# Kernel optimization log

Measured on AMD Instinct MI355X. Metric: run time of the kernel, lower is better.

## Reference

```python
import jax, jax.numpy as jnp
import numpy as np

N_NODES = 100000
N_EDGES = 1250000
D = 64


def _sage_conv(x, src, dst, W_l, b_l, W_r, n_nodes):
    # message = x[src]; scatter-mean onto dst; then lin_l(mean) + lin_r(x)
    msg = x[src]                                               # [E, D]
    agg = jax.ops.segment_sum(msg, dst, num_segments=n_nodes)  # [N, D]
    cnt = jax.ops.segment_sum(jnp.ones((src.shape[0],), x.dtype), dst,
                              num_segments=n_nodes)            # [N]
    mean = agg / jnp.maximum(cnt, 1.0)[:, None]
    return mean @ W_l + b_l + x @ W_r


def setup_inputs() -> dict:
    key = jax.random.key(0)
    ks = jax.random.split(key, 8)
    s = 1.0 / np.sqrt(D)
    x = jax.random.normal(ks[0], (N_NODES, D), dtype=jnp.float32)
    edge_index = jax.random.randint(ks[1], (2, N_EDGES), 0, N_NODES, dtype=jnp.int32)
    W_l1 = jax.random.normal(ks[2], (D, D), dtype=jnp.float32) * s
    b_l1 = jnp.zeros((D,), jnp.float32)
    W_r1 = jax.random.normal(ks[3], (D, D), dtype=jnp.float32) * s
    W_l2 = jax.random.normal(ks[4], (D, D), dtype=jnp.float32) * s
    b_l2 = jnp.zeros((D,), jnp.float32)
    W_r2 = jax.random.normal(ks[5], (D, D), dtype=jnp.float32) * s
    return {"x": x, "edge_index": edge_index,
            "W_l1": W_l1, "b_l1": b_l1, "W_r1": W_r1,
            "W_l2": W_l2, "b_l2": b_l2, "W_r2": W_r2}


def reference(x, edge_index, W_l1, b_l1, W_r1, W_l2, b_l2, W_r2):
    src, dst = edge_index[0], edge_index[1]
    n = x.shape[0]
    h = jax.nn.relu(_sage_conv(x, src, dst, W_l1, b_l1, W_r1, n))
    return _sage_conv(h, src, dst, W_l2, b_l2, W_r2, n)
```

## Files before the change

kernel.cpp:

```cpp
#include <hip/hip_runtime.h>

#define N_NODES 100000
#define N_EDGES 1250000
#define D 64

#define BIN_SHIFT 9
#define BIN_NODES 512
#define NBINS ((N_NODES + BIN_NODES - 1) >> BIN_SHIFT)
#define BIN_CAP 7168
#define SLAB 8704
#define CHUNK 4096
#define ZERO_NODE N_NODES

typedef __attribute__((ext_vector_type(8))) short short8;
typedef __attribute__((ext_vector_type(4))) float f32x4;

__device__ inline unsigned short f2bf(float f) {
    unsigned int u = __float_as_uint(f);
    unsigned int r = (u + 0x7fffu + ((u >> 16) & 1u)) >> 16;
    return (unsigned short)r;
}
__device__ inline float4 unpack_bf4(uint2 u) {
    float4 f;
    f.x = __uint_as_float(u.x << 16);
    f.y = __uint_as_float(u.x & 0xffff0000u);
    f.z = __uint_as_float(u.y << 16);
    f.w = __uint_as_float(u.y & 0xffff0000u);
    return f;
}

__global__ __launch_bounds__(256)
void convert_zero_kernel(const float4* __restrict__ xin, ushort4* __restrict__ xb,
                         int n4, int* __restrict__ bin_cnt,
                         unsigned int* __restrict__ xb_zrow,
                         unsigned int* __restrict__ h_zrow,
                         const float* __restrict__ Wl1, const float* __restrict__ Wr1,
                         const float* __restrict__ Wl2, const float* __restrict__ Wr2,
                         unsigned short* __restrict__ wt) {
    int i = blockIdx.x * 256 + threadIdx.x;
    if (i < n4) {
        float4 v = xin[i];
        ushort4 u;
        u.x = f2bf(v.x); u.y = f2bf(v.y); u.z = f2bf(v.z); u.w = f2bf(v.w);
        xb[i] = u;
    }
    if (i < NBINS) bin_cnt[i] = 0;
    if (i < 32) { xb_zrow[i] = 0u; h_zrow[i] = 0u; }
    if (i < 2 * 64 * 128) {
        int layer = i >> 13;
        int n = (i >> 7) & 63;
        int k = i & 127;
        const float* W = layer ? (k < 64 ? Wl2 : Wr2) : (k < 64 ? Wl1 : Wr1);
        float v = W[(k & 63) * D + n];
        wt[i] = f2bf(v);
    }
}

__global__ __launch_bounds__(256)
void bin_kernel(const int* __restrict__ src, const int* __restrict__ dst,
                int* __restrict__ bin_cnt, int* __restrict__ slabs) {
    __shared__ int lhist[NBINS];
    __shared__ int lstart[NBINS];
    __shared__ int lbase[NBINS];
    __shared__ int lcur[NBINS];
    __shared__ int pscan[256];
    __shared__ int sval[CHUNK];
    __shared__ int sdst[CHUNK];

    const int t = threadIdx.x;
    const int e0 = blockIdx.x * CHUNK;
    int cnt = N_EDGES - e0; if (cnt > CHUNK) cnt = CHUNK;

    for (int i = t; i < NBINS; i += 256) lhist[i] = 0;
    __syncthreads();

    for (int i = t; i < cnt; i += 256)
        atomicAdd(&lhist[dst[e0 + i] >> BIN_SHIFT], 1);
    __syncthreads();

    int h = (t < NBINS) ? lhist[t] : 0;
    pscan[t] = h;
    __syncthreads();
    for (int off = 1; off < 256; off <<= 1) {
        int x = (t >= off) ? pscan[t - off] : 0;
        __syncthreads();
        pscan[t] += x;
        __syncthreads();
    }
    if (t < NBINS) {
        int excl = pscan[t] - h;
        lstart[t] = excl;
        lcur[t] = excl;
        lbase[t] = (h > 0) ? atomicAdd(&bin_cnt[t], h) : 0;
    }
    __syncthreads();

    for (int i = t; i < cnt; i += 256) {
        int d = dst[e0 + i];
        int s = src[e0 + i];
        int b = d >> BIN_SHIFT;
        int slot = atomicAdd(&lcur[b], 1);
        int rank = slot - lstart[b];
        sval[slot] = (s << BIN_SHIFT) | (d & (BIN_NODES - 1));
        int gp = lbase[b] + rank;
        sdst[slot] = (gp < BIN_CAP) ? (b * SLAB + gp) : -1;
    }
    __syncthreads();

    for (int i = t; i < cnt; i += 256) {
        int dd = sdst[i];
        if (dd >= 0) slabs[dd] = sval[i];
    }
}

__global__ __launch_bounds__(256)
void bin_sort_kernel(int* __restrict__ slabs, const int* __restrict__ bin_cnt,
                     int* __restrict__ deg_out, int* __restrict__ rstart_out) {
    __shared__ int hist[BIN_NODES];
    __shared__ int cur[BIN_NODES];
    __shared__ int pscan[256];
    __shared__ int stage[BIN_CAP];

    const int b = blockIdx.x;
    const int t = threadIdx.x;
    int cnt = bin_cnt[b]; if (cnt > BIN_CAP) cnt = BIN_CAP;
    const int nb0 = b << BIN_SHIFT;
    const int nn = (N_NODES - nb0 < BIN_NODES) ? (N_NODES - nb0) : BIN_NODES;
    const int slab0 = b * SLAB;

    hist[t] = 0; hist[t + 256] = 0;
    __syncthreads();

    for (int i = t; i < cnt; i += 256) {
        int p = slabs[slab0 + i];
        stage[i] = p;
        atomicAdd(&hist[p & (BIN_NODES - 1)], 1);
    }
    __syncthreads();

    int h0 = hist[2 * t], h1 = hist[2 * t + 1];
    int ph0 = (h0 + 3) & ~3, ph1 = (h1 + 3) & ~3;
    int pv = ph0 + ph1;
    pscan[t] = pv;
    __syncthreads();
    for (int off = 1; off < 256; off <<= 1) {
        int x = (t >= off) ? pscan[t - off] : 0;
        __syncthreads();
        pscan[t] += x;
        __syncthreads();
    }
    int pairExcl = pscan[t] - pv;
    int s0 = pairExcl, s1 = pairExcl + ph0;
    cur[2 * t] = s0;
    cur[2 * t + 1] = s1;
    if (2 * t < nn) {
        deg_out[nb0 + 2 * t] = h0;
        rstart_out[nb0 + 2 * t] = slab0 + s0;
        for (int i = h0; i < ph0; ++i) slabs[slab0 + s0 + i] = ZERO_NODE;
    }
    if (2 * t + 1 < nn) {
        deg_out[nb0 + 2 * t + 1] = h1;
        rstart_out[nb0 + 2 * t + 1] = slab0 + s1;
        for (int i = h1; i < ph1; ++i) slabs[slab0 + s1 + i] = ZERO_NODE;
    }
    __syncthreads();

    for (int i = t; i < cnt; i += 256) {
        int p = stage[i];
        int pos = atomicAdd(&cur[p & (BIN_NODES - 1)], 1);
        slabs[slab0 + pos] = p >> BIN_SHIFT;
    }
}

template <typename TOUT>
__global__ __launch_bounds__(256, 8)
void fused_layer_kernel(const unsigned short* __restrict__ xin,
                        const int* __restrict__ rstart,
                        const int* __restrict__ deg,
                        const int* __restrict__ sorted_src,
                        const unsigned short* __restrict__ wt,
                        const float* __restrict__ bl,
                        TOUT* __restrict__ out,
                        int relu) {
    __shared__ __align__(16) unsigned short sA[32][136];

    const uint2* __restrict__ xin64 = (const uint2*)xin;

    const int tid = threadIdx.x;
    const int row0 = blockIdx.x * 32;

    const int wave = tid >> 6;
    const int lane = tid & 63;
    const int q  = lane >> 4;
    const int f2 = lane & 15;

    for (int r = wave; r < 32; r += 4) {
        int n = row0 + r;
        float4 a = make_float4(0.f, 0.f, 0.f, 0.f);
        int dg = deg[n];
        int pdg = (dg + 3) & ~3;
        int st = rstart[n];
        uint2 xraw = xin64[(size_t)n * 16 + f2];

        for (int base = 0; base < pdg; base += 64) {
            int m = pdg - base; if (m > 64) m = 64;
            int idx = 0;
            if (lane < m) idx = sorted_src[st + base + lane];
            int quads = m >> 2;
            float4 c0 = make_float4(0.f, 0.f, 0.f, 0.f);
            float4 c1 = make_float4(0.f, 0.f, 0.f, 0.f);
            float4 c2 = make_float4(0.f, 0.f, 0.f, 0.f);
            float4 c3 = make_float4(0.f, 0.f, 0.f, 0.f);
            int t = 0;
            for (; t + 4 <= quads; t += 4) {
                int sA_ = __shfl(idx, 4 * t + q);
                int sB_ = __shfl(idx, 4 * t + 4 + q);
                int sC_ = __shfl(idx, 4 * t + 8 + q);
                int sD_ = __shfl(idx, 4 * t + 12 + q);
                float4 fA = unpack_bf4(xin64[(size_t)sA_ * 16 + f2]);
                float4 fB = unpack_bf4(xin64[(size_t)sB_ * 16 + f2]);
                float4 fC = unpack_bf4(xin64[(size_t)sC_ * 16 + f2]);
                float4 fD = unpack_bf4(xin64[(size_t)sD_ * 16 + f2]);
                c0.x += fA.x; c0.y += fA.y; c0.z += fA.z; c0.w += fA.w;
                c1.x += fB.x; c1.y += fB.y; c1.z += fB.z; c1.w += fB.w;
                c2.x += fC.x; c2.y += fC.y; c2.z += fC.z; c2.w += fC.w;
                c3.x += fD.x; c3.y += fD.y; c3.z += fD.z; c3.w += fD.w;
            }
            for (; t + 2 <= quads; t += 2) {
                int sA_ = __shfl(idx, 4 * t + q);
                int sB_ = __shfl(idx, 4 * t + 4 + q);
                float4 fA = unpack_bf4(xin64[(size_t)sA_ * 16 + f2]);
                float4 fB = unpack_bf4(xin64[(size_t)sB_ * 16 + f2]);
                c0.x += fA.x; c0.y += fA.y; c0.z += fA.z; c0.w += fA.w;
                c1.x += fB.x; c1.y += fB.y; c1.z += fB.z; c1.w += fB.w;
            }
            for (; t < quads; ++t) {
                int sA_ = __shfl(idx, 4 * t + q);
                float4 fA = unpack_bf4(xin64[(size_t)sA_ * 16 + f2]);
                c0.x += fA.x; c0.y += fA.y; c0.z += fA.z; c0.w += fA.w;
            }
            a.x += (c0.x + c1.x) + (c2.x + c3.x);
            a.y += (c0.y + c1.y) + (c2.y + c3.y);
            a.z += (c0.z + c1.z) + (c2.z + c3.z);
            a.w += (c0.w + c1.w) + (c2.w + c3.w);
        }

        a.x += __shfl_xor(a.x, 16); a.y += __shfl_xor(a.y, 16);
        a.z += __shfl_xor(a.z, 16); a.w += __shfl_xor(a.w, 16);
        a.x += __shfl_xor(a.x, 32); a.y += __shfl_xor(a.y, 32);
        a.z += __shfl_xor(a.z, 32); a.w += __shfl_xor(a.w, 32);

        float inv = 1.0f / (float)(dg > 0 ? dg : 1);
        if (q == 0) {
            unsigned int p0 = (unsigned int)f2bf(a.x * inv) |
                              ((unsigned int)f2bf(a.y * inv) << 16);
            unsigned int p1 = (unsigned int)f2bf(a.z * inv) |
                              ((unsigned int)f2bf(a.w * inv) << 16);
            *(uint2*)&sA[r][f2 * 4] = make_uint2(p0, p1);
            *(uint2*)&sA[r][64 + f2 * 4] = xraw;
        }
    }
    __syncthreads();

    const int tm = wave & 1;
    const int tn0 = (wave >> 1) * 2;
    const int mrow = tm * 16 + (lane & 15);
    const int kq = (lane >> 4) * 8;

    short8 afr[4];
#pragma unroll
    for (int kk = 0; kk < 4; ++kk)
        afr[kk] = *(const short8*)&sA[mrow][kk * 32 + kq];

#pragma unroll
    for (int ti = 0; ti < 2; ++ti) {
        const int tn = tn0 + ti;
        const int col = tn * 16 + (lane & 15);
        float bias = bl[col];
        f32x4 acc = {bias, bias, bias, bias};
#pragma unroll
        for (int kk = 0; kk < 4; ++kk) {
            short8 bfr = *(const short8*)&wt[col * 128 + kk * 32 + kq];
            acc = __builtin_amdgcn_mfma_f32_16x16x32_bf16(afr[kk], bfr, acc, 0, 0, 0);
        }
        const int r0 = row0 + tm * 16 + (lane >> 4) * 4;
#pragma unroll
        for (int reg = 0; reg < 4; ++reg) {
            float o = relu ? fmaxf(acc[reg], 0.f) : acc[reg];
            if constexpr (__hip_internal::is_same<TOUT, unsigned short>::value)
                out[(size_t)(r0 + reg) * D + col] = f2bf(o);
            else
                out[(size_t)(r0 + reg) * D + col] = o;
        }
    }
}

extern "C" void kernel_launch(void* const* d_in, const int* in_sizes, int n_in,
                              void* d_out, int out_size, void* d_ws, size_t ws_size,
                              hipStream_t stream) {
    const float* x   = (const float*)d_in[0];
    const int*   ei  = (const int*)d_in[1];
    const float* Wl1 = (const float*)d_in[2];
    const float* b1  = (const float*)d_in[3];
    const float* Wr1 = (const float*)d_in[4];
    const float* Wl2 = (const float*)d_in[5];
    const float* b2  = (const float*)d_in[6];
    const float* Wr2 = (const float*)d_in[7];

    const int* src = ei;
    const int* dst = ei + N_EDGES;

    int* slabs   = (int*)d_ws;
    int* bin_cnt = slabs + (size_t)NBINS * SLAB;
    int* deg     = bin_cnt + 256;
    int* rstart  = deg + N_NODES;
    unsigned short* wt_all = (unsigned short*)(rstart + N_NODES);
    unsigned short* wt1 = wt_all;
    unsigned short* wt2 = wt_all + 64 * 128;
    unsigned short* h = wt_all + 2 * 64 * 128;
    float* out = (float*)d_out;
    unsigned short* xb = (unsigned short*)d_out;

    const int dense_blocks = N_NODES / 32;
    const int conv4 = N_NODES * D / 4;
    const int bin_blocks = (N_EDGES + CHUNK - 1) / CHUNK;

    convert_zero_kernel<<<(conv4 + 255) / 256, 256, 0, stream>>>(
        (const float4*)x, (ushort4*)xb, conv4, bin_cnt,
        (unsigned int*)(xb + (size_t)ZERO_NODE * D),
        (unsigned int*)(h + (size_t)ZERO_NODE * D),
        Wl1, Wr1, Wl2, Wr2, wt_all);

    bin_kernel<<<bin_blocks, 256, 0, stream>>>(src, dst, bin_cnt, slabs);
    bin_sort_kernel<<<NBINS, 256, 0, stream>>>(slabs, bin_cnt, deg, rstart);

    fused_layer_kernel<unsigned short><<<dense_blocks, 256, 0, stream>>>(
        xb, rstart, deg, slabs, wt1, b1, h, 1);
    fused_layer_kernel<float><<<dense_blocks, 256, 0, stream>>>(
        h, rstart, deg, slabs, wt2, b2, out, 0);
}
```

Baseline: 221.8 us.

## Replace two-pass bin sort with global atomic count, scan, and scatter CSR build

Replaces the shared-memory binning and per-bin sort of edges by destination with a standard CSR build. It counts degrees with global atomics, runs a two-level prefix scan over padded degrees, zero-fills the padding, then scatters sources using per-node atomic cursors. This removes the fixed per-bin capacity limit and the two shared-memory passes, but adds several kernel launches and many contended global atomics. Source order within each node becomes nondeterministic, so floating-point summation order can vary between runs.

```diff
diff --git a/kernel.cpp b/kernel.cpp
--- a/kernel.cpp
+++ b/kernel.cpp
@@ -3,14 +3,12 @@
 #define N_NODES 100000
 #define N_EDGES 1250000
 #define D 64
-
-#define BIN_SHIFT 9
-#define BIN_NODES 512
-#define NBINS ((N_NODES + BIN_NODES - 1) >> BIN_SHIFT)
-#define BIN_CAP 7168
-#define SLAB 8704
-#define CHUNK 4096
 #define ZERO_NODE N_NODES
+
+#define SLAB_INTS 1600000
+
+#define SCAN_BLOCKS 196
+#define SCAN_ELEMS 512
 
 typedef __attribute__((ext_vector_type(8))) short short8;
 typedef __attribute__((ext_vector_type(4))) float f32x4;
@@ -31,7 +29,7 @@
 
 __global__ __launch_bounds__(256)
 void convert_zero_kernel(const float4* __restrict__ xin, ushort4* __restrict__ xb,
-                         int n4, int* __restrict__ bin_cnt,
+                         int n4, int* __restrict__ deg,
                          unsigned int* __restrict__ xb_zrow,
                          unsigned int* __restrict__ h_zrow,
                          const float* __restrict__ Wl1, const float* __restrict__ Wr1,
@@ -44,7 +42,7 @@
         u.x = f2bf(v.x); u.y = f2bf(v.y); u.z = f2bf(v.z); u.w = f2bf(v.w);
         xb[i] = u;
     }
-    if (i < NBINS) bin_cnt[i] = 0;
+    if (i < N_NODES) deg[i] = 0;
     if (i < 32) { xb_zrow[i] = 0u; h_zrow[i] = 0u; }
     if (i < 2 * 64 * 128) {
         int layer = i >> 13;
@@ -57,90 +55,22 @@
 }
 
 __global__ __launch_bounds__(256)
-void bin_kernel(const int* __restrict__ src, const int* __restrict__ dst,
-                int* __restrict__ bin_cnt, int* __restrict__ slabs) {
-    __shared__ int lhist[NBINS];
-    __shared__ int lstart[NBINS];
-    __shared__ int lbase[NBINS];
-    __shared__ int lcur[NBINS];
+void count_kernel(const int* __restrict__ dst, int* __restrict__ deg) {
+    int i = blockIdx.x * 256 + threadIdx.x;
+    if (i < N_EDGES) atomicAdd(&deg[dst[i]], 1);
+}
+
+__global__ __launch_bounds__(256)
+void scan_block_kernel(const int* __restrict__ deg, int* __restrict__ rstart,
+                       int* __restrict__ bsum) {
     __shared__ int pscan[256];
-    __shared__ int sval[CHUNK];
-    __shared__ int sdst[CHUNK];
-
-    const int t = threadIdx.x;
-    const int e0 = blockIdx.x * CHUNK;
-    int cnt = N_EDGES - e0; if (cnt > CHUNK) cnt = CHUNK;
-
-    for (int i = t; i < NBINS; i += 256) lhist[i] = 0;
-    __syncthreads();
-
-    for (int i = t; i < cnt; i += 256)
-        atomicAdd(&lhist[dst[e0 + i] >> BIN_SHIFT], 1);
-    __syncthreads();
-
-    int h = (t < NBINS) ? lhist[t] : 0;
-    pscan[t] = h;
-    __syncthreads();
-    for (int off = 1; off < 256; off <<= 1) {
-        int x = (t >= off) ? pscan[t - off] : 0;
-        __syncthreads();
-        pscan[t] += x;
-        __syncthreads();
-    }
-    if (t < NBINS) {
-        int excl = pscan[t] - h;
-        lstart[t] = excl;
-        lcur[t] = excl;
-        lbase[t] = (h > 0) ? atomicAdd(&bin_cnt[t], h) : 0;
-    }
-    __syncthreads();
-
-    for (int i = t; i < cnt; i += 256) {
-        int d = dst[e0 + i];
-        int s = src[e0 + i];
-        int b = d >> BIN_SHIFT;
-        int slot = atomicAdd(&lcur[b], 1);
-        int rank = slot - lstart[b];
-        sval[slot] = (s << BIN_SHIFT) | (d & (BIN_NODES - 1));
-        int gp = lbase[b] + rank;
-        sdst[slot] = (gp < BIN_CAP) ? (b * SLAB + gp) : -1;
-    }
-    __syncthreads();
-
-    for (int i = t; i < cnt; i += 256) {
-        int dd = sdst[i];
-        if (dd >= 0) slabs[dd] = sval[i];
-    }
-}
-
-__global__ __launch_bounds__(256)
-void bin_sort_kernel(int* __restrict__ slabs, const int* __restrict__ bin_cnt,
-                     int* __restrict__ deg_out, int* __restrict__ rstart_out) {
-    __shared__ int hist[BIN_NODES];
-    __shared__ int cur[BIN_NODES];
-    __shared__ int pscan[256];
-    __shared__ int stage[BIN_CAP];
-
-    const int b = blockIdx.x;
-    const int t = threadIdx.x;
-    int cnt = bin_cnt[b]; if (cnt > BIN_CAP) cnt = BIN_CAP;
-    const int nb0 = b << BIN_SHIFT;
-    const int nn = (N_NODES - nb0 < BIN_NODES) ? (N_NODES - nb0) : BIN_NODES;
-    const int slab0 = b * SLAB;
-
-    hist[t] = 0; hist[t + 256] = 0;
-    __syncthreads();
-
-    for (int i = t; i < cnt; i += 256) {
-        int p = slabs[slab0 + i];
-        stage[i] = p;
-        atomicAdd(&hist[p & (BIN_NODES - 1)], 1);
-    }
-    __syncthreads();
-
-    int h0 = hist[2 * t], h1 = hist[2 * t + 1];
-    int ph0 = (h0 + 3) & ~3, ph1 = (h1 + 3) & ~3;
-    int pv = ph0 + ph1;
+    const int b = blockIdx.x, t = threadIdx.x;
+    const int i0 = b * SCAN_ELEMS + 2 * t;
+    const int i1 = i0 + 1;
+    int d0 = (i0 < N_NODES) ? deg[i0] : 0;
+    int d1 = (i1 < N_NODES) ? deg[i1] : 0;
+    int p0 = (d0 + 3) & ~3, p1 = (d1 + 3) & ~3;
+    int pv = p0 + p1;
     pscan[t] = pv;
     __syncthreads();
     for (int off = 1; off < 256; off <<= 1) {
@@ -149,26 +79,57 @@
         pscan[t] += x;
         __syncthreads();
     }
-    int pairExcl = pscan[t] - pv;
-    int s0 = pairExcl, s1 = pairExcl + ph0;
-    cur[2 * t] = s0;
-    cur[2 * t + 1] = s1;
-    if (2 * t < nn) {
-        deg_out[nb0 + 2 * t] = h0;
-        rstart_out[nb0 + 2 * t] = slab0 + s0;
-        for (int i = h0; i < ph0; ++i) slabs[slab0 + s0 + i] = ZERO_NODE;
-    }
-    if (2 * t + 1 < nn) {
-        deg_out[nb0 + 2 * t + 1] = h1;
-        rstart_out[nb0 + 2 * t + 1] = slab0 + s1;
-        for (int i = h1; i < ph1; ++i) slabs[slab0 + s1 + i] = ZERO_NODE;
-    }
+    int excl = pscan[t] - pv;
+    if (i0 < N_NODES) rstart[i0] = excl;
+    if (i1 < N_NODES) rstart[i1] = excl + p0;
+    if (t == 255) bsum[b] = pscan[255];
+}
+
+__global__ __launch_bounds__(256)
+void scan_top_kernel(const int* __restrict__ bsum, int* __restrict__ boff) {
+    __shared__ int pscan[256];
+    const int t = threadIdx.x;
+    int v = (t < SCAN_BLOCKS) ? bsum[t] : 0;
+    pscan[t] = v;
     __syncthreads();
-
-    for (int i = t; i < cnt; i += 256) {
-        int p = stage[i];
-        int pos = atomicAdd(&cur[p & (BIN_NODES - 1)], 1);
-        slabs[slab0 + pos] = p >> BIN_SHIFT;
+    for (int off = 1; off < 256; off <<= 1) {
+        int x = (t >= off) ? pscan[t - off] : 0;
+        __syncthreads();
+        pscan[t] += x;
+        __syncthreads();
+    }
+    if (t < SCAN_BLOCKS) boff[t] = pscan[t] - v;
+}
+
+__global__ __launch_bounds__(256)
+void finalize_kernel(const int* __restrict__ deg, int* __restrict__ rstart,
+                     const int* __restrict__ boff, int* __restrict__ cur,
+                     int* __restrict__ slabs) {
+    const int b = blockIdx.x, t = threadIdx.x;
+    const int off = boff[b];
+#pragma unroll
+    for (int k = 0; k < 2; ++k) {
+        int i = b * SCAN_ELEMS + t + k * 256;
+        if (i < N_NODES) {
+            int rs = rstart[i] + off;
+            rstart[i] = rs;
+            cur[i] = rs;
+            int dg = deg[i];
+            int pdg = (dg + 3) & ~3;
+            for (int j = dg; j < pdg; ++j) slabs[rs + j] = ZERO_NODE;
+        }
+    }
+}
+
+__global__ __launch_bounds__(256)
+void scatter_kernel(const int* __restrict__ src, const int* __restrict__ dst,
+                    int* __restrict__ cur, int* __restrict__ slabs) {
+    int i = blockIdx.x * 256 + threadIdx.x;
+    if (i < N_EDGES) {
+        int d = dst[i];
+        int s = src[i];
+        int pos = atomicAdd(&cur[d], 1);
+        slabs[pos] = s;
     }
 }
 
@@ -311,10 +272,12 @@
     const int* dst = ei + N_EDGES;
 
     int* slabs   = (int*)d_ws;
-    int* bin_cnt = slabs + (size_t)NBINS * SLAB;
-    int* deg     = bin_cnt + 256;
+    int* deg     = slabs + SLAB_INTS;
     int* rstart  = deg + N_NODES;
-    unsigned short* wt_all = (unsigned short*)(rstart + N_NODES);
+    int* cur     = rstart + N_NODES;
+    int* bsum    = cur + N_NODES;
+    int* boff    = bsum + 256;
+    unsigned short* wt_all = (unsigned short*)(boff + 256);
     unsigned short* wt1 = wt_all;
     unsigned short* wt2 = wt_all + 64 * 128;
     unsigned short* h = wt_all + 2 * 64 * 128;
@@ -323,16 +286,19 @@
 
     const int dense_blocks = N_NODES / 32;
     const int conv4 = N_NODES * D / 4;
-    const int bin_blocks = (N_EDGES + CHUNK - 1) / CHUNK;
+    const int edge_blocks = (N_EDGES + 255) / 256;
 
     convert_zero_kernel<<<(conv4 + 255) / 256, 256, 0, stream>>>(
-        (const float4*)x, (ushort4*)xb, conv4, bin_cnt,
+        (const float4*)x, (ushort4*)xb, conv4, deg,
         (unsigned int*)(xb + (size_t)ZERO_NODE * D),
         (unsigned int*)(h + (size_t)ZERO_NODE * D),
         Wl1, Wr1, Wl2, Wr2, wt_all);
 
-    bin_kernel<<<bin_blocks, 256, 0, stream>>>(src, dst, bin_cnt, slabs);
-    bin_sort_kernel<<<NBINS, 256, 0, stream>>>(slabs, bin_cnt, deg, rstart);
+    count_kernel<<<edge_blocks, 256, 0, stream>>>(dst, deg);
+    scan_block_kernel<<<SCAN_BLOCKS, 256, 0, stream>>>(deg, rstart, bsum);
+    scan_top_kernel<<<1, 256, 0, stream>>>(bsum, boff);
+    finalize_kernel<<<SCAN_BLOCKS, 256, 0, stream>>>(deg, rstart, boff, cur, slabs);
+    scatter_kernel<<<edge_blocks, 256, 0, stream>>>(src, dst, cur, slabs);
 
     fused_layer_kernel<unsigned short><<<dense_blocks, 256, 0, stream>>>(
         xb, rstart, deg, slabs, wt1, b1, h, 1);
```

After: 340.0 us. +53.3%, slower.

## Replace per-bin sort with global degree scan and segmented bin scatter

Applied to the files above, without the earlier changes.

Degrees are now counted with global atomics during binning, then turned into row starts by a two-level prefix scan over all nodes. The single 196-block bin_sort kernel, which used a large shared staging buffer, is replaced by a scatter kernel that runs four blocks per bin, each handling a quarter of the bin's nodes. The aim is more parallelism and occupancy in the CSR build, and a compact global layout for the sorted edge lists. In exchange it adds kernel launches and a global atomic per edge, and each scatter block re-reads the whole bin. The bin staging buffer now lives in the output buffer at an offset, which relies on that space being free at that point.

```diff
diff --git a/kernel.cpp b/kernel.cpp
--- a/kernel.cpp
+++ b/kernel.cpp
@@ -3,14 +3,18 @@
 #define N_NODES 100000
 #define N_EDGES 1250000
 #define D 64
+#define ZERO_NODE N_NODES
 
 #define BIN_SHIFT 9
 #define BIN_NODES 512
 #define NBINS ((N_NODES + BIN_NODES - 1) >> BIN_SHIFT)
 #define BIN_CAP 7168
-#define SLAB 8704
 #define CHUNK 4096
-#define ZERO_NODE N_NODES
+
+#define SLAB_INTS 1600000
+
+#define SCAN_BLOCKS 196
+#define SCAN_ELEMS 512
 
 typedef __attribute__((ext_vector_type(8))) short short8;
 typedef __attribute__((ext_vector_type(4))) float f32x4;
@@ -31,7 +35,7 @@
 
 __global__ __launch_bounds__(256)
 void convert_zero_kernel(const float4* __restrict__ xin, ushort4* __restrict__ xb,
-                         int n4, int* __restrict__ bin_cnt,
+                         int n4, int* __restrict__ deg, int* __restrict__ bin_cnt,
                          unsigned int* __restrict__ xb_zrow,
                          unsigned int* __restrict__ h_zrow,
                          const float* __restrict__ Wl1, const float* __restrict__ Wr1,
@@ -44,6 +48,7 @@
         u.x = f2bf(v.x); u.y = f2bf(v.y); u.z = f2bf(v.z); u.w = f2bf(v.w);
         xb[i] = u;
     }
+    if (i < N_NODES) deg[i] = 0;
     if (i < NBINS) bin_cnt[i] = 0;
     if (i < 32) { xb_zrow[i] = 0u; h_zrow[i] = 0u; }
     if (i < 2 * 64 * 128) {
@@ -57,8 +62,9 @@
 }
 
 __global__ __launch_bounds__(256)
-void bin_kernel(const int* __restrict__ src, const int* __restrict__ dst,
-                int* __restrict__ bin_cnt, int* __restrict__ slabs) {
+void bin_count_kernel(const int* __restrict__ src, const int* __restrict__ dst,
+                      int* __restrict__ deg, int* __restrict__ bin_cnt,
+                      int* __restrict__ binslab) {
     __shared__ int lhist[NBINS];
     __shared__ int lstart[NBINS];
     __shared__ int lbase[NBINS];
@@ -74,8 +80,11 @@
     for (int i = t; i < NBINS; i += 256) lhist[i] = 0;
     __syncthreads();
 
-    for (int i = t; i < cnt; i += 256)
-        atomicAdd(&lhist[dst[e0 + i] >> BIN_SHIFT], 1);
+    for (int i = t; i < cnt; i += 256) {
+        int d = dst[e0 + i];
+        atomicAdd(&lhist[d >> BIN_SHIFT], 1);
+        atomicAdd(&deg[d], 1);
+    }
     __syncthreads();
 
     int h = (t < NBINS) ? lhist[t] : 0;
@@ -103,44 +112,27 @@
         int rank = slot - lstart[b];
         sval[slot] = (s << BIN_SHIFT) | (d & (BIN_NODES - 1));
         int gp = lbase[b] + rank;
-        sdst[slot] = (gp < BIN_CAP) ? (b * SLAB + gp) : -1;
+        sdst[slot] = (gp < BIN_CAP) ? (b * BIN_CAP + gp) : -1;
     }
     __syncthreads();
 
     for (int i = t; i < cnt; i += 256) {
         int dd = sdst[i];
-        if (dd >= 0) slabs[dd] = sval[i];
-    }
-}
-
-__global__ __launch_bounds__(256)
-void bin_sort_kernel(int* __restrict__ slabs, const int* __restrict__ bin_cnt,
-                     int* __restrict__ deg_out, int* __restrict__ rstart_out) {
-    __shared__ int hist[BIN_NODES];
-    __shared__ int cur[BIN_NODES];
+        if (dd >= 0) binslab[dd] = sval[i];
+    }
+}
+
+__global__ __launch_bounds__(256)
+void scan_block_kernel(const int* __restrict__ deg, int* __restrict__ rstart,
+                       int* __restrict__ bsum) {
     __shared__ int pscan[256];
-    __shared__ int stage[BIN_CAP];
-
-    const int b = blockIdx.x;
-    const int t = threadIdx.x;
-    int cnt = bin_cnt[b]; if (cnt > BIN_CAP) cnt = BIN_CAP;
-    const int nb0 = b << BIN_SHIFT;
-    const int nn = (N_NODES - nb0 < BIN_NODES) ? (N_NODES - nb0) : BIN_NODES;
-    const int slab0 = b * SLAB;
-
-    hist[t] = 0; hist[t + 256] = 0;
-    __syncthreads();
-
-    for (int i = t; i < cnt; i += 256) {
-        int p = slabs[slab0 + i];
-        stage[i] = p;
-        atomicAdd(&hist[p & (BIN_NODES - 1)], 1);
-    }
-    __syncthreads();
-
-    int h0 = hist[2 * t], h1 = hist[2 * t + 1];
-    int ph0 = (h0 + 3) & ~3, ph1 = (h1 + 3) & ~3;
-    int pv = ph0 + ph1;
+    const int b = blockIdx.x, t = threadIdx.x;
+    const int i0 = b * SCAN_ELEMS + 2 * t;
+    const int i1 = i0 + 1;
+    int d0 = (i0 < N_NODES) ? deg[i0] : 0;
+    int d1 = (i1 < N_NODES) ? deg[i1] : 0;
+    int p0 = (d0 + 3) & ~3, p1 = (d1 + 3) & ~3;
+    int pv = p0 + p1;
     pscan[t] = pv;
     __syncthreads();
     for (int off = 1; off < 256; off <<= 1) {
@@ -149,26 +141,64 @@
         pscan[t] += x;
         __syncthreads();
     }
-    int pairExcl = pscan[t] - pv;
-    int s0 = pairExcl, s1 = pairExcl + ph0;
-    cur[2 * t] = s0;
-    cur[2 * t + 1] = s1;
-    if (2 * t < nn) {
-        deg_out[nb0 + 2 * t] = h0;
-        rstart_out[nb0 + 2 * t] = slab0 + s0;
-        for (int i = h0; i < ph0; ++i) slabs[slab0 + s0 + i] = ZERO_NODE;
-    }
-    if (2 * t + 1 < nn) {
-        deg_out[nb0 + 2 * t + 1] = h1;
-        rstart_out[nb0 + 2 * t + 1] = slab0 + s1;
-        for (int i = h1; i < ph1; ++i) slabs[slab0 + s1 + i] = ZERO_NODE;
-    }
-    __syncthreads();
-
+    int excl = pscan[t] - pv;
+    if (i0 < N_NODES) rstart[i0] = excl;
+    if (i1 < N_NODES) rstart[i1] = excl + p0;
+    if (t == 255) bsum[b] = pscan[255];
+}
+
+__global__ __launch_bounds__(256)
+void finalize_kernel(const int* __restrict__ deg, int* __restrict__ rstart,
+                     const int* __restrict__ bsum, int* __restrict__ slabs) {
+    __shared__ int pscan[256];
+    __shared__ int boff[SCAN_BLOCKS];
+    const int t = threadIdx.x;
+    int v = (t < SCAN_BLOCKS) ? bsum[t] : 0;
+    pscan[t] = v;
+    __syncthreads();
+    for (int off = 1; off < 256; off <<= 1) {
+        int x = (t >= off) ? pscan[t - off] : 0;
+        __syncthreads();
+        pscan[t] += x;
+        __syncthreads();
+    }
+    if (t < SCAN_BLOCKS) boff[t] = pscan[t] - v;
+    __syncthreads();
+
+    int i = blockIdx.x * 256 + t;
+    if (i < N_NODES) {
+        int rs = rstart[i] + boff[i >> BIN_SHIFT];
+        rstart[i] = rs;
+        int dg = deg[i];
+        int pdg = (dg + 3) & ~3;
+        for (int j = dg; j < pdg; ++j) slabs[rs + j] = ZERO_NODE;
+    }
+}
+
+__global__ __launch_bounds__(256)
+void bin_scatter_kernel(const int* __restrict__ binslab,
+                        const int* __restrict__ bin_cnt,
+                        const int* __restrict__ rstart,
+                        int* __restrict__ slabs) {
+    __shared__ int cur[128];
+    const int b = blockIdx.x >> 2;
+    const int seg = blockIdx.x & 3;
+    const int t = threadIdx.x;
+    const int nb0 = (b << BIN_SHIFT) + (seg << 7);
+    if (t < 128) {
+        int n = nb0 + t;
+        cur[t] = (n < N_NODES) ? rstart[n] : 0;
+    }
+    __syncthreads();
+    int cnt = bin_cnt[b]; if (cnt > BIN_CAP) cnt = BIN_CAP;
+    const int s0 = b * BIN_CAP;
     for (int i = t; i < cnt; i += 256) {
-        int p = stage[i];
-        int pos = atomicAdd(&cur[p & (BIN_NODES - 1)], 1);
-        slabs[slab0 + pos] = p >> BIN_SHIFT;
+        int p = binslab[s0 + i];
+        int dlow = p & (BIN_NODES - 1);
+        if ((dlow >> 7) == seg) {
+            int pos = atomicAdd(&cur[dlow & 127], 1);
+            slabs[pos] = p >> BIN_SHIFT;
+        }
     }
 }
 
@@ -311,28 +341,33 @@
     const int* dst = ei + N_EDGES;
 
     int* slabs   = (int*)d_ws;
-    int* bin_cnt = slabs + (size_t)NBINS * SLAB;
-    int* deg     = bin_cnt + 256;
+    int* deg     = slabs + SLAB_INTS;
     int* rstart  = deg + N_NODES;
-    unsigned short* wt_all = (unsigned short*)(rstart + N_NODES);
+    int* bin_cnt = rstart + N_NODES;
+    int* bsum    = bin_cnt + 256;
+    unsigned short* wt_all = (unsigned short*)(bsum + 256);
     unsigned short* wt1 = wt_all;
     unsigned short* wt2 = wt_all + 64 * 128;
     unsigned short* h = wt_all + 2 * 64 * 128;
     float* out = (float*)d_out;
     unsigned short* xb = (unsigned short*)d_out;
+    int* binslab = (int*)d_out + 4 * 1024 * 1024;
 
     const int dense_blocks = N_NODES / 32;
     const int conv4 = N_NODES * D / 4;
     const int bin_blocks = (N_EDGES + CHUNK - 1) / CHUNK;
+    const int fin_blocks = (N_NODES + 255) / 256;
 
     convert_zero_kernel<<<(conv4 + 255) / 256, 256, 0, stream>>>(
-        (const float4*)x, (ushort4*)xb, conv4, bin_cnt,
+        (const float4*)x, (ushort4*)xb, conv4, deg, bin_cnt,
         (unsigned int*)(xb + (size_t)ZERO_NODE * D),
         (unsigned int*)(h + (size_t)ZERO_NODE * D),
         Wl1, Wr1, Wl2, Wr2, wt_all);
 
-    bin_kernel<<<bin_blocks, 256, 0, stream>>>(src, dst, bin_cnt, slabs);
-    bin_sort_kernel<<<NBINS, 256, 0, stream>>>(slabs, bin_cnt, deg, rstart);
+    bin_count_kernel<<<bin_blocks, 256, 0, stream>>>(src, dst, deg, bin_cnt, binslab);
+    scan_block_kernel<<<SCAN_BLOCKS, 256, 0, stream>>>(deg, rstart, bsum);
+    finalize_kernel<<<fin_blocks, 256, 0, stream>>>(deg, rstart, bsum, slabs);
+    bin_scatter_kernel<<<NBINS * 4, 256, 0, stream>>>(binslab, bin_cnt, rstart, slabs);
 
     fused_layer_kernel<unsigned short><<<dense_blocks, 256, 0, stream>>>(
         xb, rstart, deg, slabs, wt1, b1, h, 1);
```

New measurement: 270.6 us. +22.0%, slower.

## Split bin sort across four blocks per bin and use wave-shuffle scans

Applied to the files above, without the earlier changes.

The per-bin sort is split into four blocks, each owning a quarter of the bin's destination nodes. Each block recomputes the bin histogram and scan, then scatters only its own edges, which gives more parallelism than one block per bin. The partition step now writes into a separate staging buffer placed inside the output buffer, uses smaller chunks (more blocks), and replaces the shared-memory scan with a wave-shuffle scan. In exchange, every bin's edges are read four times, and the staging buffer reuses the output region before the final layer overwrites it.

```diff
diff --git a/kernel.cpp b/kernel.cpp
--- a/kernel.cpp
+++ b/kernel.cpp
@@ -3,14 +3,16 @@
 #define N_NODES 100000
 #define N_EDGES 1250000
 #define D 64
+#define ZERO_NODE N_NODES
 
 #define BIN_SHIFT 9
 #define BIN_NODES 512
 #define NBINS ((N_NODES + BIN_NODES - 1) >> BIN_SHIFT)
 #define BIN_CAP 7168
-#define SLAB 8704
-#define CHUNK 4096
-#define ZERO_NODE N_NODES
+#define BIN_SLAB 8704
+#define CHUNK 2048
+
+#define SLAB_INTS (NBINS * BIN_SLAB)
 
 typedef __attribute__((ext_vector_type(8))) short short8;
 typedef __attribute__((ext_vector_type(4))) float f32x4;
@@ -57,17 +59,18 @@
 }
 
 __global__ __launch_bounds__(256)
-void bin_kernel(const int* __restrict__ src, const int* __restrict__ dst,
-                int* __restrict__ bin_cnt, int* __restrict__ slabs) {
+void bin_partition_kernel(const int* __restrict__ src, const int* __restrict__ dst,
+                          int* __restrict__ bin_cnt, int* __restrict__ binslab) {
     __shared__ int lhist[NBINS];
     __shared__ int lstart[NBINS];
     __shared__ int lbase[NBINS];
     __shared__ int lcur[NBINS];
-    __shared__ int pscan[256];
+    __shared__ int wsum[4];
     __shared__ int sval[CHUNK];
     __shared__ int sdst[CHUNK];
 
     const int t = threadIdx.x;
+    const int lane = t & 63, wave = t >> 6;
     const int e0 = blockIdx.x * CHUNK;
     int cnt = N_EDGES - e0; if (cnt > CHUNK) cnt = CHUNK;
 
@@ -79,16 +82,17 @@
     __syncthreads();
 
     int h = (t < NBINS) ? lhist[t] : 0;
-    pscan[t] = h;
-    __syncthreads();
-    for (int off = 1; off < 256; off <<= 1) {
-        int x = (t >= off) ? pscan[t - off] : 0;
-        __syncthreads();
-        pscan[t] += x;
-        __syncthreads();
-    }
+    int v = h;
+    for (int off = 1; off < 64; off <<= 1) {
+        int u = __shfl_up(v, off);
+        if (lane >= off) v += u;
+    }
+    if (lane == 63) wsum[wave] = v;
+    __syncthreads();
+    int wpre = 0;
+    for (int w = 0; w < wave; ++w) wpre += wsum[w];
     if (t < NBINS) {
-        int excl = pscan[t] - h;
+        int excl = v + wpre - h;
         lstart[t] = excl;
         lcur[t] = excl;
         lbase[t] = (h > 0) ? atomicAdd(&bin_cnt[t], h) : 0;
@@ -103,72 +107,77 @@
         int rank = slot - lstart[b];
         sval[slot] = (s << BIN_SHIFT) | (d & (BIN_NODES - 1));
         int gp = lbase[b] + rank;
-        sdst[slot] = (gp < BIN_CAP) ? (b * SLAB + gp) : -1;
+        sdst[slot] = (gp < BIN_CAP) ? (b * BIN_CAP + gp) : -1;
     }
     __syncthreads();
 
     for (int i = t; i < cnt; i += 256) {
         int dd = sdst[i];
-        if (dd >= 0) slabs[dd] = sval[i];
+        if (dd >= 0) binslab[dd] = sval[i];
     }
 }
 
 __global__ __launch_bounds__(256)
-void bin_sort_kernel(int* __restrict__ slabs, const int* __restrict__ bin_cnt,
-                     int* __restrict__ deg_out, int* __restrict__ rstart_out) {
+void seg_build_kernel(const int* __restrict__ binslab, const int* __restrict__ bin_cnt,
+                      int* __restrict__ deg_out, int* __restrict__ rstart_out,
+                      int* __restrict__ slabs) {
     __shared__ int hist[BIN_NODES];
-    __shared__ int cur[BIN_NODES];
-    __shared__ int pscan[256];
-    __shared__ int stage[BIN_CAP];
-
-    const int b = blockIdx.x;
+    __shared__ int lcur[128];
+    __shared__ int wsum[4];
+
+    const int b = blockIdx.x >> 2;
+    const int seg = blockIdx.x & 3;
     const int t = threadIdx.x;
+    const int lane = t & 63, wave = t >> 6;
     int cnt = bin_cnt[b]; if (cnt > BIN_CAP) cnt = BIN_CAP;
+    const int s0 = b * BIN_CAP;
     const int nb0 = b << BIN_SHIFT;
-    const int nn = (N_NODES - nb0 < BIN_NODES) ? (N_NODES - nb0) : BIN_NODES;
-    const int slab0 = b * SLAB;
 
     hist[t] = 0; hist[t + 256] = 0;
     __syncthreads();
 
+    for (int i = t; i < cnt; i += 256)
+        atomicAdd(&hist[binslab[s0 + i] & (BIN_NODES - 1)], 1);
+    __syncthreads();
+
+    int h0 = hist[2 * t], h1 = hist[2 * t + 1];
+    int p0 = (h0 + 3) & ~3, p1 = (h1 + 3) & ~3;
+    int pv = p0 + p1;
+    int v = pv;
+    for (int off = 1; off < 64; off <<= 1) {
+        int u = __shfl_up(v, off);
+        if (lane >= off) v += u;
+    }
+    if (lane == 63) wsum[wave] = v;
+    __syncthreads();
+    int wpre = 0;
+    for (int w = 0; w < wave; ++w) wpre += wsum[w];
+    int pairExcl = v + wpre - pv;
+
+    if (wave == seg) {
+        int rs0 = b * BIN_SLAB + pairExcl;
+        int rs1 = rs0 + p0;
+        int n0 = nb0 + 2 * t, n1 = n0 + 1;
+        if (n0 < N_NODES) {
+            deg_out[n0] = h0; rstart_out[n0] = rs0;
+            for (int j = h0; j < p0; ++j) slabs[rs0 + j] = ZERO_NODE;
+        }
+        if (n1 < N_NODES) {
+            deg_out[n1] = h1; rstart_out[n1] = rs1;
+            for (int j = h1; j < p1; ++j) slabs[rs1 + j] = ZERO_NODE;
+        }
+        lcur[(2 * t) & 127] = rs0;
+        lcur[(2 * t + 1) & 127] = rs1;
+    }
+    __syncthreads();
+
     for (int i = t; i < cnt; i += 256) {
-        int p = slabs[slab0 + i];
-        stage[i] = p;
-        atomicAdd(&hist[p & (BIN_NODES - 1)], 1);
-    }
-    __syncthreads();
-
-    int h0 = hist[2 * t], h1 = hist[2 * t + 1];
-    int ph0 = (h0 + 3) & ~3, ph1 = (h1 + 3) & ~3;
-    int pv = ph0 + ph1;
-    pscan[t] = pv;
-    __syncthreads();
-    for (int off = 1; off < 256; off <<= 1) {
-        int x = (t >= off) ? pscan[t - off] : 0;
-        __syncthreads();
-        pscan[t] += x;
-        __syncthreads();
-    }
-    int pairExcl = pscan[t] - pv;
-    int s0 = pairExcl, s1 = pairExcl + ph0;
-    cur[2 * t] = s0;
-    cur[2 * t + 1] = s1;
-    if (2 * t < nn) {
-        deg_out[nb0 + 2 * t] = h0;
-        rstart_out[nb0 + 2 * t] = slab0 + s0;
-        for (int i = h0; i < ph0; ++i) slabs[slab0 + s0 + i] = ZERO_NODE;
-    }
-    if (2 * t + 1 < nn) {
-        deg_out[nb0 + 2 * t + 1] = h1;
-        rstart_out[nb0 + 2 * t + 1] = slab0 + s1;
-        for (int i = h1; i < ph1; ++i) slabs[slab0 + s1 + i] = ZERO_NODE;
-    }
-    __syncthreads();
-
-    for (int i = t; i < cnt; i += 256) {
-        int p = stage[i];
-        int pos = atomicAdd(&cur[p & (BIN_NODES - 1)], 1);
-        slabs[slab0 + pos] = p >> BIN_SHIFT;
+        int p = binslab[s0 + i];
+        int dlow = p & (BIN_NODES - 1);
+        if ((dlow >> 7) == seg) {
+            int pos = atomicAdd(&lcur[dlow & 127], 1);
+            slabs[pos] = p >> BIN_SHIFT;
+        }
     }
 }
 
@@ -311,19 +320,20 @@
     const int* dst = ei + N_EDGES;
 
     int* slabs   = (int*)d_ws;
-    int* bin_cnt = slabs + (size_t)NBINS * SLAB;
-    int* deg     = bin_cnt + 256;
+    int* deg     = slabs + SLAB_INTS;
     int* rstart  = deg + N_NODES;
-    unsigned short* wt_all = (unsigned short*)(rstart + N_NODES);
+    int* bin_cnt = rstart + N_NODES;
+    unsigned short* wt_all = (unsigned short*)(bin_cnt + 256);
     unsigned short* wt1 = wt_all;
     unsigned short* wt2 = wt_all + 64 * 128;
     unsigned short* h = wt_all + 2 * 64 * 128;
     float* out = (float*)d_out;
     unsigned short* xb = (unsigned short*)d_out;
+    int* binslab = (int*)d_out + 4 * 1024 * 1024;
 
     const int dense_blocks = N_NODES / 32;
     const int conv4 = N_NODES * D / 4;
-    const int bin_blocks = (N_EDGES + CHUNK - 1) / CHUNK;
+    const int part_blocks = (N_EDGES + CHUNK - 1) / CHUNK;
 
     convert_zero_kernel<<<(conv4 + 255) / 256, 256, 0, stream>>>(
         (const float4*)x, (ushort4*)xb, conv4, bin_cnt,
@@ -331,8 +341,8 @@
         (unsigned int*)(h + (size_t)ZERO_NODE * D),
         Wl1, Wr1, Wl2, Wr2, wt_all);
 
-    bin_kernel<<<bin_blocks, 256, 0, stream>>>(src, dst, bin_cnt, slabs);
-    bin_sort_kernel<<<NBINS, 256, 0, stream>>>(slabs, bin_cnt, deg, rstart);
+    bin_partition_kernel<<<part_blocks, 256, 0, stream>>>(src, dst, bin_cnt, binslab);
+    seg_build_kernel<<<NBINS * 4, 256, 0, stream>>>(binslab, bin_cnt, deg, rstart, slabs);
 
     fused_layer_kernel<unsigned short><<<dense_blocks, 256, 0, stream>>>(
         xb, rstart, deg, slabs, wt1, b1, h, 1);
```

Result: slower. 228.0 us (+2.8%).
